# Kernel tuning notes

Measured on AMD Instinct MI355X. Metric: run time of the kernel, lower is better.

Reference implementation:

```python
import jax, jax.numpy as jnp
import numpy as np

PAD = -999            # PADDING_INDEX sentinel from madrax
B, M = 4, 4096        # structures, atom slots per structure
N = B * M             # total atoms
CUTOFF = 7.0          # distance_threshold default in get_pairwise_representation
BOX = 80.0            # Angstrom box -> realistic neighbor density


def setup_inputs() -> dict:
    key = jax.random.key(0)
    k1, k2, k3, k4, k5, k6 = jax.random.split(key, 6)
    coordinates = jax.random.uniform(k1, (B, M, 3), jnp.float32) * BOX
    # pad the last 128 atom slots of every structure (coords[...,0] == PAD marks padding)
    coordinates = coordinates.at[:, M - 128:, 0].set(float(PAD))
    atom_batch = (jnp.arange(N) // M).astype(jnp.int32)                     # atom_description[:,0]
    coords_indexing_atom = jax.random.randint(k2, (N,), 0, M, jnp.int32)    # irregular gather slots
    partners = jax.random.randint(k3, (N, 2), 0, M, jnp.int32)
    partners = jnp.where(jax.random.uniform(k4, (N, 2)) < 0.1, PAD, partners)
    angle_indices = jax.random.randint(k5, (N, 4), 0, N, jnp.int32)
    angle_indices = jnp.where(jax.random.uniform(k6, (N, 1)) < 0.2, PAD, angle_indices)
    return {
        "coordinates": coordinates,
        "atom_batch": atom_batch,
        "coords_indexing_atom": coords_indexing_atom,
        "partners_indexing_atom": partners,
        "angle_indices": angle_indices,
    }


def _dihedral(p1, p2, p3, p4):
    # math_utils.dihedral2dVectors: standard signed torsion angle
    b1, b2, b3 = p2 - p1, p3 - p2, p4 - p3
    n1 = jnp.cross(b1, b2)
    n2 = jnp.cross(b2, b3)
    b2n = b2 / (jnp.linalg.norm(b2, axis=-1, keepdims=True) + 1e-12)
    m1 = jnp.cross(n1, b2n)
    x = jnp.sum(n1 * n2, axis=-1)
    y = jnp.sum(m1 * n2, axis=-1)
    return jnp.arctan2(y, x)


def reference(coordinates, atom_batch, coords_indexing_atom, partners_indexing_atom, angle_indices):
    # --- gather atom coordinates (coords = coordinates[batch, slot]) ---
    coords = coordinates[atom_batch, coords_indexing_atom]                   # [N,3]

    # --- gather partner coordinates with PAD masking (partners_final) ---
    pvalid = partners_indexing_atom != PAD                                   # [N,2]
    safe_p = jnp.where(pvalid, partners_indexing_atom, 0)
    pcoords = coordinates[atom_batch[:, None], safe_p]                       # [N,2,3]
    partners_final = jnp.where(pvalid[..., None], pcoords, float(PAD))

    # --- per-batch pairwise distance + 7A cutoff (get_pairwise_representation) ---
    cb = coords.reshape(B, M, 3)
    valid = cb[..., 0] != float(PAD)                                         # [B,M]
    sq = jnp.sum(cb * cb, axis=-1)                                           # [B,M]
    d2 = sq[:, :, None] + sq[:, None, :] - 2.0 * jnp.einsum('bic,bjc->bij', cb, cb)
    dist = jnp.sqrt(jnp.maximum(d2, 0.0) + 1e-12)                            # [B,M,M]
    pair_mask = valid[:, :, None] & valid[:, None, :] & (dist <= CUTOFF)
    # fixed-shape surrogate for the ragged pair list: per-atom neighbor distance sum
    nbr_sum = jnp.sum(jnp.where(pair_mask, dist, 0.0), axis=-1).reshape(N)   # [N]

    # --- dihedral angles with padding mask (_calculate_angles) ---
    amask = jnp.all(angle_indices != PAD, axis=-1)                           # [N]
    aidx = jnp.where(amask[:, None], angle_indices, 0)
    p = coords[aidx]                                                          # [N,4,3]
    ang = _dihedral(p[:, 0], p[:, 1], p[:, 2], p[:, 3])
    angles = jnp.where(amask, ang, float(PAD))                               # [N]

    # pack outputs: [N, 8] = angle, neighbor-dist-sum, partner coords (2x3)
    return jnp.concatenate([angles[:, None], nbr_sum[:, None], partners_final.reshape(N, 6)], axis=-1)
```

## Files before the change

kernel.cpp:

```cpp
#include <hip/hip_runtime.h>
#include <math.h>

#define kB 4
#define kM 4096
#define kN (kB * kM)
#define kPadF -999.0f
#define kPadI -999

__device__ __forceinline__ float sq_np(float x, float y, float z) {
    return __fadd_rn(__fadd_rn(__fmul_rn(x, x), __fmul_rn(y, y)),
                     __fmul_rn(z, z));
}

__device__ __forceinline__ float fast_sqrt(float x) {
#if __has_builtin(__builtin_amdgcn_sqrtf)
    return __builtin_amdgcn_sqrtf(x);
#else
    float r;
    asm volatile("v_sqrt_f32 %0, %1" : "=v"(r) : "v"(x));
    return r;
#endif
}

__global__ __launch_bounds__(64)
void per_atom_kernel(const float* __restrict__ coords,
                     const int*   __restrict__ cidx,
                     const int*   __restrict__ partners,
                     const int*   __restrict__ aidx,
                     float*       __restrict__ out,
                     float4*      __restrict__ ws)
{
    int i = blockIdx.x * 64 + threadIdx.x;
    if (i >= kN) return;
    int b = i >> 12;

    {
        int gc = cidx[i];
        const float* s = coords + (size_t)(b * kM + gc) * 3;
        float x = s[0], y = s[1], z = s[2];
        ws[i] = make_float4(x, y, z, sq_np(x, y, z));
    }

    float o2, o3, o4, o5, o6, o7;
    int p0 = partners[2 * i + 0];
    int p1 = partners[2 * i + 1];
    if (p0 == kPadI) { o2 = o3 = o4 = kPadF; }
    else {
        const float* s = coords + (size_t)(b * kM + p0) * 3;
        o2 = s[0]; o3 = s[1]; o4 = s[2];
    }
    if (p1 == kPadI) { o5 = o6 = o7 = kPadF; }
    else {
        const float* s = coords + (size_t)(b * kM + p1) * 3;
        o5 = s[0]; o6 = s[1]; o7 = s[2];
    }

    int4 a = *reinterpret_cast<const int4*>(aidx + 4 * i);
    float ang = kPadF;
    if (a.x != kPadI && a.y != kPadI && a.z != kPadI && a.w != kPadI) {
        int ai[4] = {a.x, a.y, a.z, a.w};
        float P[4][3];
        #pragma unroll
        for (int k = 0; k < 4; ++k) {
            int g  = ai[k];
            int gb = g >> 12;
            int gc = cidx[g];
            const float* s = coords + (size_t)(gb * kM + gc) * 3;
            P[k][0] = s[0]; P[k][1] = s[1]; P[k][2] = s[2];
        }
        float b1x = P[1][0] - P[0][0], b1y = P[1][1] - P[0][1], b1z = P[1][2] - P[0][2];
        float b2x = P[2][0] - P[1][0], b2y = P[2][1] - P[1][1], b2z = P[2][2] - P[1][2];
        float b3x = P[3][0] - P[2][0], b3y = P[3][1] - P[2][1], b3z = P[3][2] - P[2][2];
        float n1x = b1y * b2z - b1z * b2y;
        float n1y = b1z * b2x - b1x * b2z;
        float n1z = b1x * b2y - b1y * b2x;
        float n2x = b2y * b3z - b2z * b3y;
        float n2y = b2z * b3x - b2x * b3z;
        float n2z = b2x * b3y - b2y * b3x;
        float nb2 = sqrtf(b2x * b2x + b2y * b2y + b2z * b2z) + 1e-12f;
        float inv = 1.0f / nb2;
        float ux = b2x * inv, uy = b2y * inv, uz = b2z * inv;
        float m1x = n1y * uz - n1z * uy;
        float m1y = n1z * ux - n1x * uz;
        float m1z = n1x * uy - n1y * ux;
        float x = n1x * n2x + n1y * n2y + n1z * n2z;
        float y = m1x * n2x + m1y * n2y + m1z * n2z;
        ang = atan2f(y, x);
    }

    float4* o = reinterpret_cast<float4*>(out + (size_t)i * 8);
    o[0] = make_float4(ang, 0.0f, o2, o3);
    o[1] = make_float4(o4, o5, o6, o7);
}

__global__ __launch_bounds__(256)
void nbr_kernel(const float4* __restrict__ ws,
                float*        __restrict__ out)
{
    __shared__ float4 sc[64];

    int rowBlk = blockIdx.x >> 6;
    int colChk = blockIdx.x & 63;
    int row0   = rowBlk << 10;
    int b      = rowBlk >> 2;
    int col0   = colChk << 6;

    int tid = threadIdx.x;
    if (tid < 64) sc[tid] = ws[(size_t)b * kM + col0 + tid];
    __syncthreads();

    float rx[4], ry[4], rz[4], rsq[4], sum[4];
    bool  rv[4];
    #pragma unroll
    for (int k = 0; k < 4; ++k) {
        float4 ci = ws[row0 + tid + (k << 8)];
        rx[k] = ci.x; ry[k] = ci.y; rz[k] = ci.z; rsq[k] = ci.w;
        rv[k] = (ci.x != kPadF);
        sum[k] = 0.0f;
    }

    for (int j = 0; j < 64; j += 4) {
        float4 cc0 = sc[j + 0], cc1 = sc[j + 1], cc2 = sc[j + 2], cc3 = sc[j + 3];
        #pragma unroll
        for (int u = 0; u < 4; ++u) {
            float4 c = (u == 0) ? cc0 : (u == 1) ? cc1 : (u == 2) ? cc2 : cc3;
            #pragma unroll
            for (int k = 0; k < 4; ++k) {
                float dot = __fmaf_rn(rz[k], c.z,
                            __fmaf_rn(ry[k], c.y, __fmul_rn(rx[k], c.x)));
                float d2  = __fsub_rn(__fadd_rn(rsq[k], c.w),
                                      __fmul_rn(2.0f, dot));
                bool  in  = (d2 <= 49.0f);
                if (__any(in)) {
                    float d2m  = __fadd_rn(fmaxf(d2, 0.0f), 1e-12f);
                    float dist = fast_sqrt(d2m);
                    sum[k] += in ? dist : 0.0f;
                }
            }
        }
    }

    #pragma unroll
    for (int k = 0; k < 4; ++k) {
        if (rv[k] && sum[k] != 0.0f) {
            atomicAdd(out + (size_t)(row0 + tid + (k << 8)) * 8 + 1, sum[k]);
        }
    }
}

__global__ __launch_bounds__(256)
void nbr_kernel_lds(const float* __restrict__ coords,
                    const int*   __restrict__ cidx,
                    float*       __restrict__ out)
{
    __shared__ float4 sc[kM];
    int b    = blockIdx.x >> 6;
    int row0 = (blockIdx.x & 63) << 6;
    for (int j = threadIdx.x; j < kM; j += 256) {
        int idx = cidx[b * kM + j];
        const float* s = coords + (size_t)(b * kM + idx) * 3;
        float x = s[0], y = s[1], z = s[2];
        sc[j] = make_float4(x, y, z, sq_np(x, y, z));
    }
    __syncthreads();
    int r   = row0 + (threadIdx.x >> 2);
    int sub = threadIdx.x & 3;
    float4 ci = sc[r];
    float sum = 0.0f;
    for (int jj = 0; jj < kM / 4; ++jj) {
        float4 c   = sc[4 * jj + sub];
        float dot  = __fmaf_rn(ci.z, c.z,
                     __fmaf_rn(ci.y, c.y, __fmul_rn(ci.x, c.x)));
        float d2   = __fsub_rn(__fadd_rn(ci.w, c.w), __fmul_rn(2.0f, dot));
        bool  in   = (d2 <= 49.0f);
        if (__any(in)) {
            float d2m  = __fadd_rn(fmaxf(d2, 0.0f), 1e-12f);
            float dist = fast_sqrt(d2m);
            sum += in ? dist : 0.0f;
        }
    }
    sum += __shfl_xor(sum, 1);
    sum += __shfl_xor(sum, 2);
    if (sub == 0)
        out[(size_t)(b * kM + r) * 8 + 1] = (ci.x != kPadF) ? sum : 0.0f;
}

extern "C" void kernel_launch(void* const* d_in, const int* in_sizes, int n_in,
                              void* d_out, int out_size, void* d_ws, size_t ws_size,
                              hipStream_t stream) {
    const float* coords   = (const float*)d_in[0];
    const int*   cidx     = (const int*)d_in[2];
    const int*   partners = (const int*)d_in[3];
    const int*   aidx     = (const int*)d_in[4];
    float*       out      = (float*)d_out;
    float4*      ws       = (float4*)d_ws;

    hipLaunchKernelGGL(per_atom_kernel, dim3(kN / 64), dim3(64), 0, stream,
                       coords, cidx, partners, aidx, out, ws);

    if (ws_size >= (size_t)kN * sizeof(float4)) {
        hipLaunchKernelGGL(nbr_kernel, dim3(1024), dim3(256), 0, stream,
                           ws, out);
    } else {
        hipLaunchKernelGGL(nbr_kernel_lds, dim3(kB * 64), dim3(256), 0, stream,
                           coords, cidx, out);
    }
}
```

Measured before the change: 81.93 us.

## Exploit distance symmetry with upper-triangular tiles and LDS column-sum atomics

```diff
diff --git a/kernel.cpp b/kernel.cpp
--- a/kernel.cpp
+++ b/kernel.cpp
@@ -94,56 +94,56 @@
 }
 
 __global__ __launch_bounds__(256)
-void nbr_kernel(const float4* __restrict__ ws,
-                float*        __restrict__ out)
+void nbr_sym_kernel(const float4* __restrict__ ws,
+                    float*        __restrict__ out)
 {
-    __shared__ float4 sc[64];
-
-    int rowBlk = blockIdx.x >> 6;
-    int colChk = blockIdx.x & 63;
-    int row0   = rowBlk << 10;
-    int b      = rowBlk >> 2;
-    int col0   = colChk << 6;
-
+    __shared__ float4 sc[256];
+    __shared__ float  colsum[256];
+
+    int blk = blockIdx.x;
+    int b   = blk / 136;
+    int t   = blk - b * 136;
+    int tr  = 0;
+    while (t >= 16 - tr) { t -= 16 - tr; ++tr; }
+    int tc  = tr + t;
+    bool diag = (tc == tr);
+
+    const float4* base = ws + (size_t)b * kM;
     int tid = threadIdx.x;
-    if (tid < 64) sc[tid] = ws[(size_t)b * kM + col0 + tid];
+
+    sc[tid]     = base[tc * 256 + tid];
+    colsum[tid] = 0.0f;
+    float4 ri   = base[tr * 256 + tid];
     __syncthreads();
 
-    float rx[4], ry[4], rz[4], rsq[4], sum[4];
-    bool  rv[4];
-    #pragma unroll
-    for (int k = 0; k < 4; ++k) {
-        float4 ci = ws[row0 + tid + (k << 8)];
-        rx[k] = ci.x; ry[k] = ci.y; rz[k] = ci.z; rsq[k] = ci.w;
-        rv[k] = (ci.x != kPadF);
-        sum[k] = 0.0f;
-    }
-
-    for (int j = 0; j < 64; j += 4) {
+    float rowsum = 0.0f;
+    for (int j = 0; j < 256; j += 4) {
         float4 cc0 = sc[j + 0], cc1 = sc[j + 1], cc2 = sc[j + 2], cc3 = sc[j + 3];
         #pragma unroll
         for (int u = 0; u < 4; ++u) {
             float4 c = (u == 0) ? cc0 : (u == 1) ? cc1 : (u == 2) ? cc2 : cc3;
-            #pragma unroll
-            for (int k = 0; k < 4; ++k) {
-                float dot = __fmaf_rn(rz[k], c.z,
-                            __fmaf_rn(ry[k], c.y, __fmul_rn(rx[k], c.x)));
-                float d2  = __fsub_rn(__fadd_rn(rsq[k], c.w),
-                                      __fmul_rn(2.0f, dot));
-                bool  in  = (d2 <= 49.0f);
-                if (__any(in)) {
-                    float d2m  = __fadd_rn(fmaxf(d2, 0.0f), 1e-12f);
-                    float dist = fast_sqrt(d2m);
-                    sum[k] += in ? dist : 0.0f;
+            float dot = __fmaf_rn(ri.z, c.z,
+                        __fmaf_rn(ri.y, c.y, __fmul_rn(ri.x, c.x)));
+            float d2  = __fmaf_rn(-2.0f, dot, __fadd_rn(ri.w, c.w));
+            bool  in  = (d2 <= 49.0f);
+            if (__any(in)) {
+                float dist = fast_sqrt(__fadd_rn(fmaxf(d2, 0.0f), 1e-12f));
+                rowsum += in ? dist : 0.0f;
+                if (!diag && in) {
+                    atomicAdd(&colsum[j + u], dist);
                 }
             }
         }
     }
-
-    #pragma unroll
-    for (int k = 0; k < 4; ++k) {
-        if (rv[k] && sum[k] != 0.0f) {
-            atomicAdd(out + (size_t)(row0 + tid + (k << 8)) * 8 + 1, sum[k]);
+    __syncthreads();
+
+    if (ri.x != kPadF && rowsum != 0.0f) {
+        atomicAdd(out + (size_t)(b * kM + tr * 256 + tid) * 8 + 1, rowsum);
+    }
+    if (!diag) {
+        float cs = colsum[tid];
+        if (cs != 0.0f && sc[tid].x != kPadF) {
+            atomicAdd(out + (size_t)(b * kM + tc * 256 + tid) * 8 + 1, cs);
         }
     }
 }
@@ -171,11 +171,10 @@
         float4 c   = sc[4 * jj + sub];
         float dot  = __fmaf_rn(ci.z, c.z,
                      __fmaf_rn(ci.y, c.y, __fmul_rn(ci.x, c.x)));
-        float d2   = __fsub_rn(__fadd_rn(ci.w, c.w), __fmul_rn(2.0f, dot));
+        float d2   = __fmaf_rn(-2.0f, dot, __fadd_rn(ci.w, c.w));
         bool  in   = (d2 <= 49.0f);
         if (__any(in)) {
-            float d2m  = __fadd_rn(fmaxf(d2, 0.0f), 1e-12f);
-            float dist = fast_sqrt(d2m);
+            float dist = fast_sqrt(__fadd_rn(fmaxf(d2, 0.0f), 1e-12f));
             sum += in ? dist : 0.0f;
         }
     }
@@ -199,7 +198,7 @@
                        coords, cidx, partners, aidx, out, ws);
 
     if (ws_size >= (size_t)kN * sizeof(float4)) {
-        hipLaunchKernelGGL(nbr_kernel, dim3(1024), dim3(256), 0, stream,
+        hipLaunchKernelGGL(nbr_sym_kernel, dim3(kB * 136), dim3(256), 0, stream,
                            ws, out);
     } else {
         hipLaunchKernelGGL(nbr_kernel_lds, dim3(kB * 64), dim3(256), 0, stream,
```

Result: no change. 82.68 us (+0.9%).
